# Performance work log

Measured on AMD Instinct MI355X. Metric: run time of the kernel, lower is better.

Reference implementation:

```python
import jax, jax.numpy as jnp
import numpy as np

B, S, C = 8, 512, 1024
H = 16
R = 32            # lora_rank
LORA_ALPHA = 1.0  # lora scaling (alpha=1)
HID = C           # mlp_ratio = 1


def setup_inputs() -> dict:
    key = jax.random.key(0)
    ks = jax.random.split(key, 20)
    g = lambda k, shp, s=0.02: jax.random.normal(k, shp, dtype=jnp.float32) * s
    inp = {
        "x": jax.random.normal(ks[0], (B, S, C), dtype=jnp.float32),
        "mask": jax.random.randint(ks[1], (B, 3 * S), 0, 2).astype(bool),
        # qkv: Linear(dim, 3*dim, bias=False), stored [in, out]
        "qkv_w": g(ks[2], (C, 3 * C)),
        "qkv_la": g(ks[3], (C, R)),
        "qkv_lb": g(ks[4], (R, 3 * C)),
        "proj_w": g(ks[5], (C, C)),
        "proj_b": jnp.zeros((C,), jnp.float32),
        "proj_la": g(ks[6], (C, R)),
        "proj_lb": g(ks[7], (R, C)),
        "fc1_w": g(ks[8], (C, HID)),
        "fc1_b": jnp.zeros((HID,), jnp.float32),
        "fc1_la": g(ks[9], (C, R)),
        "fc1_lb": g(ks[10], (R, HID)),
        "fc2_w": g(ks[11], (HID, C)),
        "fc2_b": jnp.zeros((C,), jnp.float32),
        "fc2_la": g(ks[12], (C, R)),
        "fc2_lb": g(ks[13], (R, C)),
    }
    return inp


def reference(x, mask, qkv_w, qkv_la, qkv_lb, proj_w, proj_b, proj_la, proj_lb,
              fc1_w, fc1_b, fc1_la, fc1_lb, fc2_w, fc2_b, fc2_la, fc2_lb):
    # cross_modality='a', mask_modality='a' (constants)
    b, s, c = x.shape
    hd = c // H
    scale = hd ** (-0.5)

    # fused QKV + LoRA low-rank update
    qkv = x @ qkv_w + ((x @ qkv_la) @ qkv_lb) * LORA_ALPHA      # [B,S,3C]
    qkv = qkv.reshape(b, s, 3, H, hd).transpose(2, 0, 3, 1, 4)  # [3,B,H,S,hd]
    q, k, v = qkv[0] * scale, qkv[1], qkv[2]

    # fp32 QK^T, modality 'a' mask slice, fill -inf, softmax, NaN->0
    attn = jnp.einsum('bhqd,bhkd->bhqk',
                      q.astype(jnp.float32), k.astype(jnp.float32))
    m = mask[:, :s]                                             # 'a' slice
    attn = jnp.where(m[:, None, None, :], attn, -jnp.inf)
    attn = jax.nn.softmax(attn, axis=-1).astype(x.dtype)
    attn = jnp.where(jnp.isnan(attn), jnp.zeros((), x.dtype), attn)

    xo = jnp.einsum('bhqk,bhkd->bhqd', attn, v)                 # [B,H,S,hd]
    xo = xo.transpose(0, 2, 1, 3).reshape(b, s, c)

    # MLP (with LoRA on both fc layers); torch nn.GELU default = exact erf
    h = xo @ fc1_w + fc1_b + ((xo @ fc1_la) @ fc1_lb) * LORA_ALPHA
    h = jax.nn.gelu(h, approximate=False)
    h = h @ fc2_w + fc2_b + ((h @ fc2_la) @ fc2_lb) * LORA_ALPHA
    xo = xo + h

    out = xo @ proj_w + proj_b + ((xo @ proj_la) @ proj_lb) * LORA_ALPHA
    return out
```

## Files before the change

### kernel.cpp

```cpp
#include <hip/hip_runtime.h>

typedef _Float16 f16;
typedef _Float16 f16x8 __attribute__((ext_vector_type(8)));
typedef _Float16 f16x4v __attribute__((ext_vector_type(4)));
typedef float f32x4 __attribute__((ext_vector_type(4)));

#define DEVINL __device__ __forceinline__

DEVINL void gload16(const void* g, void* l) {
  __builtin_amdgcn_global_load_lds(
      (const __attribute__((address_space(1))) void*)g,
      (__attribute__((address_space(3))) void*)l, 16, 0, 0);
}

__global__ __launch_bounds__(256) void weff3(
    const float* __restrict__ W, const float* __restrict__ la,
    const float* __restrict__ lb, f16* __restrict__ WT,
    int N, int K, int scaleCols)
{
  __shared__ float La[64][36];
  __shared__ f16 Ts[64][72];
  int t = threadIdx.x;
  int n0 = blockIdx.x * 64, k0 = blockIdx.y * 64;
  int w = t >> 6, nn = t & 63;
  #pragma unroll
  for (int i = 0; i < 8; ++i) {
    int idx = i * 256 + t;
    int row = idx >> 5, r = idx & 31;
    La[row][r] = la[(size_t)(k0 + row) * 32 + r];
  }
  float lbr[32];
  #pragma unroll
  for (int r = 0; r < 32; ++r) lbr[r] = lb[(size_t)r * N + n0 + nn];
  float scale = (n0 + nn < scaleCols) ? 0.125f : 1.0f;
  __syncthreads();
  float prev = 0.0f;
  #pragma unroll
  for (int i = 0; i < 16; ++i) {
    int k = w * 16 + i;
    float acc = W[(size_t)(k0 + k) * N + n0 + nn];
    #pragma unroll
    for (int rc = 0; rc < 8; ++rc) {
      float4 a4 = *(const float4*)&La[k][rc * 4];
      acc += a4.x * lbr[rc * 4] + a4.y * lbr[rc * 4 + 1] +
             a4.z * lbr[rc * 4 + 2] + a4.w * lbr[rc * 4 + 3];
    }
    acc *= scale;
    if (i & 1) {
      union { f16 h[2]; unsigned u; } pk;
      pk.h[0] = (f16)prev; pk.h[1] = (f16)acc;
      *(unsigned*)&Ts[nn][k - 1] = pk.u;
    } else prev = acc;
  }
  __syncthreads();
  #pragma unroll
  for (int it = 0; it < 2; ++it) {
    int id = it * 256 + t;
    int row = id >> 3, c8 = id & 7;
    f16x8 h = *(const f16x8*)&Ts[row][c8 * 8];
    *(f16x8*)(WT + (size_t)(n0 + row) * K + k0 + c8 * 8) = h;
  }
}

__global__ __launch_bounds__(256) void cvt_f32_f16(const float* __restrict__ in,
                                                   f16* __restrict__ out)
{
  int i = (blockIdx.x * 256 + threadIdx.x) * 4;
  float4 v = *(const float4*)(in + i);
  f16x4v o = {(f16)v.x, (f16)v.y, (f16)v.z, (f16)v.w};
  *(f16x4v*)(out + i) = o;
}

__global__ __launch_bounds__(256) void mask_canon(const unsigned char* __restrict__ m,
                                                  unsigned char* __restrict__ out)
{
  __shared__ int flag;
  if (threadIdx.x == 0) flag = 0;
  __syncthreads();
  int found = 0;
  for (int p = threadIdx.x; p < 12288; p += 256)
    if ((p & 3) && m[p]) found = 1;
  if (found) flag = 1;
  __syncthreads();
  int u8 = flag;
  const int* mi = (const int*)m;
  for (int idx = threadIdx.x; idx < 4096; idx += 256) {
    int b = idx >> 9, k = idx & 511;
    int v = u8 ? (int)m[b * 1536 + k] : mi[b * 1536 + k];
    out[idx] = (unsigned char)(v != 0);
  }
}

template <int EPI>
__global__ __launch_bounds__(256) void gemm128(
    const f16* __restrict__ A, const f16* __restrict__ Bt,
    int M, int N, int K,
    const float* __restrict__ bias, const f16* __restrict__ resid,
    f16* __restrict__ outH, float* __restrict__ outF,
    f16* __restrict__ Qo, f16* __restrict__ Ko, f16* __restrict__ Vto)
{
  __shared__ __align__(16) f16 As[2][128 * 64];
  __shared__ __align__(16) f16 Bs[2][128 * 64];
  int tid = threadIdx.x, wid = tid >> 6, l = tid & 63;
  int lg = l >> 4, lr = l & 15;
  int nbx = gridDim.x;
  int nwg = nbx * gridDim.y;
  int flat = blockIdx.y * nbx + blockIdx.x;
  flat = (flat & 7) * (nwg >> 3) + (flat >> 3);
  int bm = (flat % nbx) * 128, bn = (flat / nbx) * 128;
  int wr = (wid >> 1) * 64, wc = (wid & 1) * 64;
  f32x4 acc[4][4] = {};

  int srow = l >> 3, scol = l & 7;
  int sc8 = (scol ^ srow) * 8;
  const f16* gA = A + (size_t)(bm + wid * 32 + srow) * K + sc8;
  const f16* gB = Bt + (size_t)(bn + wid * 32 + srow) * K + sc8;
  int lo = wid * 32 * 64;

  #pragma unroll
  for (int is = 0; is < 4; ++is) {
    gload16(gA + (size_t)(is * 8) * K, As[0] + lo + is * 8 * 64);
    gload16(gB + (size_t)(is * 8) * K, Bs[0] + lo + is * 8 * 64);
  }
  __syncthreads();

  int nt = K >> 6;
  for (int ts = 0; ts < nt; ++ts) {
    int cur = ts & 1, nxt = cur ^ 1;
    if (ts + 1 < nt) {
      int k1 = (ts + 1) << 6;
      #pragma unroll
      for (int is = 0; is < 4; ++is) {
        gload16(gA + (size_t)(is * 8) * K + k1, As[nxt] + lo + is * 8 * 64);
        gload16(gB + (size_t)(is * 8) * K + k1, Bs[nxt] + lo + is * 8 * 64);
      }
    }
    const f16* Ac = As[cur];
    const f16* Bc = Bs[cur];
    f16x8 af[2][4], bf[2][4];
    int x = lr & 7;
    #pragma unroll
    for (int i = 0; i < 4; ++i) {
      int row = wr + i * 16 + lr;
      af[0][i] = *(const f16x8*)(Ac + row * 64 + ((lg ^ x) * 8));
      af[1][i] = *(const f16x8*)(Ac + row * 64 + (((4 + lg) ^ x) * 8));
    }
    #pragma unroll
    for (int j = 0; j < 4; ++j) {
      int row = wc + j * 16 + lr;
      bf[0][j] = *(const f16x8*)(Bc + row * 64 + ((lg ^ x) * 8));
      bf[1][j] = *(const f16x8*)(Bc + row * 64 + (((4 + lg) ^ x) * 8));
    }
    #pragma unroll
    for (int kk = 0; kk < 2; ++kk)
      #pragma unroll
      for (int i = 0; i < 4; ++i)
        #pragma unroll
        for (int j = 0; j < 4; ++j)
          acc[i][j] = __builtin_amdgcn_mfma_f32_16x16x32_f16(af[kk][i], bf[kk][j], acc[i][j], 0, 0, 0);
    __syncthreads();
  }

  #pragma unroll
  for (int i = 0; i < 4; ++i) {
    #pragma unroll
    for (int j = 0; j < 4; ++j) {
      int n = bn + wc + j * 16 + lr;
      float bv = (EPI >= 1) ? bias[n] : 0.0f;
      #pragma unroll
      for (int r = 0; r < 4; ++r) {
        int m = bm + wr + i * 16 + lg * 4 + r;
        float v = acc[i][j][r];
        if (EPI == 0) {
          int bb = m >> 9, ss = m & 511;
          int which = n >> 10, c = n & 1023, hh = c >> 6, dd = c & 63;
          size_t base = (size_t)(bb * 16 + hh);
          if (which == 0)      Qo[(base * 512 + ss) * 64 + dd] = (f16)v;
          else if (which == 1) Ko[(base * 512 + ss) * 64 + dd] = (f16)v;
          else                 Vto[(base * 64 + dd) * 512 + ss] = (f16)v;
        } else if (EPI == 1) {
          v += bv;
          v = 0.5f * v * (1.0f + erff(v * 0.70710678118654752f));
          outH[(size_t)m * N + n] = (f16)v;
        } else if (EPI == 2) {
          v += bv + (float)resid[(size_t)m * N + n];
          outH[(size_t)m * N + n] = (f16)v;
        } else {
          outF[(size_t)m * N + n] = v + bv;
        }
      }
    }
  }
}

__global__ __launch_bounds__(256) void attn_kernel(
    const f16* __restrict__ Q, const f16* __restrict__ Kc,
    const f16* __restrict__ Vt, const unsigned char* __restrict__ cmask,
    f16* __restrict__ XO)
{
  __shared__ __align__(16) f16 Ks[128 * 64];
  __shared__ __align__(16) f16 Vs[64 * 128];
  __shared__ __align__(16) f16 Ps[4 * 32 * 128];
  int tid = threadIdx.x, w = tid >> 6, l = tid & 63;
  int lg = l >> 4, lr = l & 15;
  int flat = blockIdx.y * 4 + blockIdx.x;
  flat = (flat & 7) * 64 + (flat >> 3);
  int qblk = flat & 3, bh = flat >> 2;
  int b = bh >> 4, h = bh & 15;
  const f16* Qg = Q + (size_t)bh * 512 * 64 + qblk * 128 * 64;
  const f16* Kg = Kc + (size_t)bh * 512 * 64;
  const f16* Vg = Vt + (size_t)bh * 64 * 512;
  const unsigned char* mb = cmask + b * 512;

  f16x8 qf[2][2];
  #pragma unroll
  for (int i = 0; i < 2; ++i)
    #pragma unroll
    for (int kc = 0; kc < 2; ++kc)
      qf[i][kc] = *(const f16x8*)(Qg + (size_t)(w * 32 + i * 16 + lr) * 64 + kc * 32 + lg * 8);

  f32x4 O[2][4] = {};
  float mrow[2][4], lrow[2][4];
  #pragma unroll
  for (int i = 0; i < 2; ++i)
    #pragma unroll
    for (int r = 0; r < 4; ++r) { mrow[i][r] = -1e30f; lrow[i][r] = 0.0f; }

  f16* Pw = Ps + w * 32 * 128;
  int ksrow = l >> 3;
  int ksc = ((l & 7) ^ ksrow) * 8;
  int vrow = l >> 4;
  int v7 = (w * 4 + vrow) & 7;
  int vsc = ((l & 15) ^ v7) * 8;

  for (int kt = 0; kt < 4; ++kt) {
    __syncthreads();
    #pragma unroll
    for (int is = 0; is < 4; ++is)
      gload16(Kg + (size_t)(kt * 128 + is * 32 + w * 8 + ksrow) * 64 + ksc,
              Ks + (is * 32 + w * 8) * 64);
    #pragma unroll
    for (int is = 0; is < 4; ++is)
      gload16(Vg + (size_t)(is * 16 + w * 4 + vrow) * 512 + kt * 128 + vsc,
              Vs + (is * 16 + w * 4) * 128);
    __syncthreads();

    int x = lr & 7;
    f32x4 sc[2][8] = {};
    #pragma unroll
    for (int j = 0; j < 8; ++j) {
      const f16* krow = Ks + (j * 16 + lr) * 64;
      f16x8 kf0 = *(const f16x8*)(krow + ((lg ^ x) * 8));
      f16x8 kf1 = *(const f16x8*)(krow + (((4 + lg) ^ x) * 8));
      sc[0][j] = __builtin_amdgcn_mfma_f32_16x16x32_f16(qf[0][0], kf0, sc[0][j], 0, 0, 0);
      sc[0][j] = __builtin_amdgcn_mfma_f32_16x16x32_f16(qf[0][1], kf1, sc[0][j], 0, 0, 0);
      sc[1][j] = __builtin_amdgcn_mfma_f32_16x16x32_f16(qf[1][0], kf0, sc[1][j], 0, 0, 0);
      sc[1][j] = __builtin_amdgcn_mfma_f32_16x16x32_f16(qf[1][1], kf1, sc[1][j], 0, 0, 0);
    }
    bool keep[8];
    #pragma unroll
    for (int j = 0; j < 8; ++j) keep[j] = mb[kt * 128 + j * 16 + lr] != 0;
    #pragma unroll
    for (int i = 0; i < 2; ++i)
      #pragma unroll
      for (int j = 0; j < 8; ++j)
        #pragma unroll
        for (int r = 0; r < 4; ++r)
          sc[i][j][r] = keep[j] ? sc[i][j][r] : -1e30f;

    #pragma unroll
    for (int i = 0; i < 2; ++i) {
      #pragma unroll
      for (int r = 0; r < 4; ++r) {
        float pm = sc[i][0][r];
        #pragma unroll
        for (int j = 1; j < 8; ++j) pm = fmaxf(pm, sc[i][j][r]);
        pm = fmaxf(pm, __shfl_xor(pm, 1));
        pm = fmaxf(pm, __shfl_xor(pm, 2));
        pm = fmaxf(pm, __shfl_xor(pm, 4));
        pm = fmaxf(pm, __shfl_xor(pm, 8));
        float mn = fmaxf(mrow[i][r], pm);
        float alpha = __expf(mrow[i][r] - mn);
        mrow[i][r] = mn;
        lrow[i][r] *= alpha;
        #pragma unroll
        for (int jd = 0; jd < 4; ++jd) O[i][jd][r] *= alpha;
      }
    }
    #pragma unroll
    for (int i = 0; i < 2; ++i) {
      float rs[4] = {0.f, 0.f, 0.f, 0.f};
      #pragma unroll
      for (int j = 0; j < 8; ++j)
        #pragma unroll
        for (int r = 0; r < 4; ++r) {
          float p = __expf(sc[i][j][r] - mrow[i][r]);
          rs[r] += p;
          int prow = i * 16 + lg * 4 + r;
          int pc = j * 16 + lr;
          Pw[prow * 128 + ((((pc >> 3) ^ (prow & 7)) << 3) | (pc & 7))] = (f16)p;
        }
      #pragma unroll
      for (int r = 0; r < 4; ++r) {
        float s = rs[r];
        s += __shfl_xor(s, 1); s += __shfl_xor(s, 2);
        s += __shfl_xor(s, 4); s += __shfl_xor(s, 8);
        lrow[i][r] += s;
      }
    }
    #pragma unroll
    for (int kk = 0; kk < 4; ++kk) {
      int c0 = ((kk * 4 + lg) ^ x) * 8;
      f16x8 pa0 = *(const f16x8*)(Pw + lr * 128 + c0);
      f16x8 pa1 = *(const f16x8*)(Pw + (16 + lr) * 128 + c0);
      #pragma unroll
      for (int jd = 0; jd < 4; ++jd) {
        f16x8 vb = *(const f16x8*)(Vs + (jd * 16 + lr) * 128 + c0);
        O[0][jd] = __builtin_amdgcn_mfma_f32_16x16x32_f16(pa0, vb, O[0][jd], 0, 0, 0);
        O[1][jd] = __builtin_amdgcn_mfma_f32_16x16x32_f16(pa1, vb, O[1][jd], 0, 0, 0);
      }
    }
  }

  #pragma unroll
  for (int i = 0; i < 2; ++i)
    #pragma unroll
    for (int r = 0; r < 4; ++r) {
      int q = qblk * 128 + w * 32 + i * 16 + lg * 4 + r;
      float inv = 1.0f / lrow[i][r];
      #pragma unroll
      for (int jd = 0; jd < 4; ++jd) {
        int c = h * 64 + jd * 16 + lr;
        XO[((size_t)b * 512 + q) * 1024 + c] = (f16)(O[i][jd][r] * inv);
      }
    }
}

extern "C" void kernel_launch(void* const* d_in, const int* in_sizes, int n_in,
                              void* d_out, int out_size, void* d_ws, size_t ws_size,
                              hipStream_t stream)
{
  (void)in_sizes; (void)n_in; (void)out_size; (void)ws_size;
  const float* x            = (const float*)d_in[0];
  const unsigned char* mask = (const unsigned char*)d_in[1];
  const float* qkv_w   = (const float*)d_in[2];
  const float* qkv_la  = (const float*)d_in[3];
  const float* qkv_lb  = (const float*)d_in[4];
  const float* proj_w  = (const float*)d_in[5];
  const float* proj_b  = (const float*)d_in[6];
  const float* proj_la = (const float*)d_in[7];
  const float* proj_lb = (const float*)d_in[8];
  const float* fc1_w   = (const float*)d_in[9];
  const float* fc1_b   = (const float*)d_in[10];
  const float* fc1_la  = (const float*)d_in[11];
  const float* fc1_lb  = (const float*)d_in[12];
  const float* fc2_w   = (const float*)d_in[13];
  const float* fc2_b   = (const float*)d_in[14];
  const float* fc2_la  = (const float*)d_in[15];
  const float* fc2_lb  = (const float*)d_in[16];
  float* out = (float*)d_out;

  f16* p = (f16*)d_ws;
  f16* WqkvT = p; p += 3072 * 1024;
  f16* W1T   = p; p += 1024 * 1024;
  f16* W2T   = p; p += 1024 * 1024;
  f16* WpT   = p; p += 1024 * 1024;
  f16* Xh    = p; p += 4096 * 1024;
  f16* Qb    = p; p += 128 * 512 * 64;
  f16* Kb    = p; p += 128 * 512 * 64;
  f16* Vt    = p; p += 128 * 64 * 512;
  f16* XO    = p; p += 4096 * 1024;
  unsigned char* cmask = (unsigned char*)p;
  f16* Hb  = Qb;
  f16* XO2 = Xh;

  weff3<<<dim3(48, 16), 256, 0, stream>>>(qkv_w, qkv_la, qkv_lb, WqkvT, 3072, 1024, 1024);
  weff3<<<dim3(16, 16), 256, 0, stream>>>(fc1_w, fc1_la, fc1_lb, W1T, 1024, 1024, 0);
  weff3<<<dim3(16, 16), 256, 0, stream>>>(fc2_w, fc2_la, fc2_lb, W2T, 1024, 1024, 0);
  weff3<<<dim3(16, 16), 256, 0, stream>>>(proj_w, proj_la, proj_lb, WpT, 1024, 1024, 0);
  cvt_f32_f16<<<4096, 256, 0, stream>>>(x, Xh);
  mask_canon<<<1, 256, 0, stream>>>(mask, cmask);

  gemm128<0><<<dim3(32, 24), 256, 0, stream>>>(Xh, WqkvT, 4096, 3072, 1024,
      nullptr, nullptr, nullptr, nullptr, Qb, Kb, Vt);
  attn_kernel<<<dim3(4, 128), 256, 0, stream>>>(Qb, Kb, Vt, cmask, XO);
  gemm128<1><<<dim3(32, 8), 256, 0, stream>>>(XO, W1T, 4096, 1024, 1024,
      fc1_b, nullptr, Hb, nullptr, nullptr, nullptr, nullptr);
  gemm128<2><<<dim3(32, 8), 256, 0, stream>>>(Hb, W2T, 4096, 1024, 1024,
      fc2_b, XO, XO2, nullptr, nullptr, nullptr, nullptr);
  gemm128<3><<<dim3(32, 8), 256, 0, stream>>>(XO2, WpT, 4096, 1024, 1024,
      proj_b, nullptr, nullptr, out, nullptr, nullptr, nullptr);
}
```

Before: 314.4 us.

## Retile GEMMs with BK=32 and BM template, register-prefetch attention K/V

The GEMM is templated on BM with a K-step of 32 instead of 64, which shrinks LDS use and allows three blocks per CU. The three 1024-wide GEMMs switch to 64-row tiles so they launch twice as many workgroups. The XCD-aware block remap is changed, and s_setprio is raised around the MFMA loops. The attention kernel now prefetches the next K/V tile into registers and writes it to swizzled LDS, replacing direct global-to-LDS loads, and gets a two-blocks-per-CU launch bound. Halving the K-step doubles the number of barriers per GEMM, and the smaller tiles reduce data reuse per block.

```diff
diff --git a/kernel.cpp b/kernel.cpp
--- a/kernel.cpp
+++ b/kernel.cpp
@@ -91,78 +91,76 @@
   }
 }
 
-template <int EPI>
-__global__ __launch_bounds__(256) void gemm128(
+template <int EPI, int BM>
+__global__ __launch_bounds__(256, 3) void gemmk(
     const f16* __restrict__ A, const f16* __restrict__ Bt,
     int M, int N, int K,
     const float* __restrict__ bias, const f16* __restrict__ resid,
     f16* __restrict__ outH, float* __restrict__ outF,
     f16* __restrict__ Qo, f16* __restrict__ Ko, f16* __restrict__ Vto)
 {
-  __shared__ __align__(16) f16 As[2][128 * 64];
-  __shared__ __align__(16) f16 Bs[2][128 * 64];
+  constexpr int MF = BM / 32;
+  __shared__ __align__(16) f16 As[2][BM * 32];
+  __shared__ __align__(16) f16 Bs[2][128 * 32];
   int tid = threadIdx.x, wid = tid >> 6, l = tid & 63;
   int lg = l >> 4, lr = l & 15;
   int nbx = gridDim.x;
-  int nwg = nbx * gridDim.y;
   int flat = blockIdx.y * nbx + blockIdx.x;
-  flat = (flat & 7) * (nwg >> 3) + (flat >> 3);
-  int bm = (flat % nbx) * 128, bn = (flat / nbx) * 128;
-  int wr = (wid >> 1) * 64, wc = (wid & 1) * 64;
-  f32x4 acc[4][4] = {};
-
-  int srow = l >> 3, scol = l & 7;
-  int sc8 = (scol ^ srow) * 8;
-  const f16* gA = A + (size_t)(bm + wid * 32 + srow) * K + sc8;
-  const f16* gB = Bt + (size_t)(bn + wid * 32 + srow) * K + sc8;
-  int lo = wid * 32 * 64;
-
-  #pragma unroll
-  for (int is = 0; is < 4; ++is) {
-    gload16(gA + (size_t)(is * 8) * K, As[0] + lo + is * 8 * 64);
-    gload16(gB + (size_t)(is * 8) * K, Bs[0] + lo + is * 8 * 64);
-  }
+  int xcd = flat & 7, idx = flat >> 3;
+  int mc = nbx >> 3;
+  int bm = (xcd * mc + idx % mc) * BM;
+  int bn = (idx / mc) * 128;
+  int wr = (wid >> 1) * (BM / 2), wc = (wid & 1) * 64;
+  f32x4 acc[MF][4] = {};
+
+  int swz = ((l & 3) ^ ((l >> 3) & 3)) * 8;
+  const f16* gA = A + (size_t)(bm + wid * (BM / 4) + (l >> 2)) * K + swz;
+  const f16* gB = Bt + (size_t)(bn + wid * 32 + (l >> 2)) * K + swz;
+  int xr = (lr >> 1) & 3;
+
+  #pragma unroll
+  for (int ig = 0; ig < BM / 64; ++ig)
+    gload16(gA + (size_t)(ig * 16) * K, As[0] + (wid * (BM / 4) + ig * 16) * 32);
+  #pragma unroll
+  for (int ig = 0; ig < 2; ++ig)
+    gload16(gB + (size_t)(ig * 16) * K, Bs[0] + (wid * 32 + ig * 16) * 32);
   __syncthreads();
 
-  int nt = K >> 6;
+  int nt = K >> 5;
   for (int ts = 0; ts < nt; ++ts) {
     int cur = ts & 1, nxt = cur ^ 1;
     if (ts + 1 < nt) {
-      int k1 = (ts + 1) << 6;
-      #pragma unroll
-      for (int is = 0; is < 4; ++is) {
-        gload16(gA + (size_t)(is * 8) * K + k1, As[nxt] + lo + is * 8 * 64);
-        gload16(gB + (size_t)(is * 8) * K + k1, Bs[nxt] + lo + is * 8 * 64);
-      }
+      int k1 = (ts + 1) << 5;
+      #pragma unroll
+      for (int ig = 0; ig < BM / 64; ++ig)
+        gload16(gA + (size_t)(ig * 16) * K + k1, As[nxt] + (wid * (BM / 4) + ig * 16) * 32);
+      #pragma unroll
+      for (int ig = 0; ig < 2; ++ig)
+        gload16(gB + (size_t)(ig * 16) * K + k1, Bs[nxt] + (wid * 32 + ig * 16) * 32);
     }
     const f16* Ac = As[cur];
     const f16* Bc = Bs[cur];
-    f16x8 af[2][4], bf[2][4];
-    int x = lr & 7;
-    #pragma unroll
-    for (int i = 0; i < 4; ++i) {
-      int row = wr + i * 16 + lr;
-      af[0][i] = *(const f16x8*)(Ac + row * 64 + ((lg ^ x) * 8));
-      af[1][i] = *(const f16x8*)(Ac + row * 64 + (((4 + lg) ^ x) * 8));
-    }
+    f16x8 bf[4];
     #pragma unroll
     for (int j = 0; j < 4; ++j) {
       int row = wc + j * 16 + lr;
-      bf[0][j] = *(const f16x8*)(Bc + row * 64 + ((lg ^ x) * 8));
-      bf[1][j] = *(const f16x8*)(Bc + row * 64 + (((4 + lg) ^ x) * 8));
-    }
-    #pragma unroll
-    for (int kk = 0; kk < 2; ++kk)
-      #pragma unroll
-      for (int i = 0; i < 4; ++i)
-        #pragma unroll
-        for (int j = 0; j < 4; ++j)
-          acc[i][j] = __builtin_amdgcn_mfma_f32_16x16x32_f16(af[kk][i], bf[kk][j], acc[i][j], 0, 0, 0);
+      bf[j] = *(const f16x8*)(Bc + row * 32 + ((lg ^ xr) * 8));
+    }
+    __builtin_amdgcn_s_setprio(1);
+    #pragma unroll
+    for (int i = 0; i < MF; ++i) {
+      int row = wr + i * 16 + lr;
+      f16x8 af = *(const f16x8*)(Ac + row * 32 + ((lg ^ xr) * 8));
+      #pragma unroll
+      for (int j = 0; j < 4; ++j)
+        acc[i][j] = __builtin_amdgcn_mfma_f32_16x16x32_f16(af, bf[j], acc[i][j], 0, 0, 0);
+    }
+    __builtin_amdgcn_s_setprio(0);
     __syncthreads();
   }
 
   #pragma unroll
-  for (int i = 0; i < 4; ++i) {
+  for (int i = 0; i < MF; ++i) {
     #pragma unroll
     for (int j = 0; j < 4; ++j) {
       int n = bn + wc + j * 16 + lr;
@@ -193,7 +191,7 @@
   }
 }
 
-__global__ __launch_bounds__(256) void attn_kernel(
+__global__ __launch_bounds__(256, 2) void attn_kernel(
     const f16* __restrict__ Q, const f16* __restrict__ Kc,
     const f16* __restrict__ Vt, const unsigned char* __restrict__ cmask,
     f16* __restrict__ XO)
@@ -227,26 +225,36 @@
     for (int r = 0; r < 4; ++r) { mrow[i][r] = -1e30f; lrow[i][r] = 0.0f; }
 
   f16* Pw = Ps + w * 32 * 128;
-  int ksrow = l >> 3;
-  int ksc = ((l & 7) ^ ksrow) * 8;
-  int vrow = l >> 4;
-  int v7 = (w * 4 + vrow) & 7;
-  int vsc = ((l & 15) ^ v7) * 8;
+
+  int kR = tid >> 3, kC = (tid & 7) * 8;
+  int vR = tid >> 4, vC = (tid & 15) * 8;
+  f16x8 kreg[4], vreg[4];
+  #pragma unroll
+  for (int i = 0; i < 4; ++i) {
+    kreg[i] = *(const f16x8*)(Kg + (size_t)(i * 32 + kR) * 64 + kC);
+    vreg[i] = *(const f16x8*)(Vg + (size_t)(i * 16 + vR) * 512 + vC);
+  }
 
   for (int kt = 0; kt < 4; ++kt) {
+    #pragma unroll
+    for (int i = 0; i < 4; ++i) {
+      int krow = i * 32 + kR;
+      *(f16x8*)(Ks + krow * 64 + (((tid & 7) ^ (krow & 7)) * 8)) = kreg[i];
+      int vrow = i * 16 + vR;
+      *(f16x8*)(Vs + vrow * 128 + (((tid & 15) ^ (vrow & 7)) * 8)) = vreg[i];
+    }
     __syncthreads();
-    #pragma unroll
-    for (int is = 0; is < 4; ++is)
-      gload16(Kg + (size_t)(kt * 128 + is * 32 + w * 8 + ksrow) * 64 + ksc,
-              Ks + (is * 32 + w * 8) * 64);
-    #pragma unroll
-    for (int is = 0; is < 4; ++is)
-      gload16(Vg + (size_t)(is * 16 + w * 4 + vrow) * 512 + kt * 128 + vsc,
-              Vs + (is * 16 + w * 4) * 128);
-    __syncthreads();
+    if (kt < 3) {
+      #pragma unroll
+      for (int i = 0; i < 4; ++i) {
+        kreg[i] = *(const f16x8*)(Kg + (size_t)((kt + 1) * 128 + i * 32 + kR) * 64 + kC);
+        vreg[i] = *(const f16x8*)(Vg + (size_t)(i * 16 + vR) * 512 + (kt + 1) * 128 + vC);
+      }
+    }
 
     int x = lr & 7;
     f32x4 sc[2][8] = {};
+    __builtin_amdgcn_s_setprio(1);
     #pragma unroll
     for (int j = 0; j < 8; ++j) {
       const f16* krow = Ks + (j * 16 + lr) * 64;
@@ -257,6 +265,7 @@
       sc[1][j] = __builtin_amdgcn_mfma_f32_16x16x32_f16(qf[1][0], kf0, sc[1][j], 0, 0, 0);
       sc[1][j] = __builtin_amdgcn_mfma_f32_16x16x32_f16(qf[1][1], kf1, sc[1][j], 0, 0, 0);
     }
+    __builtin_amdgcn_s_setprio(0);
     bool keep[8];
     #pragma unroll
     for (int j = 0; j < 8; ++j) keep[j] = mb[kt * 128 + j * 16 + lr] != 0;
@@ -308,6 +317,7 @@
         lrow[i][r] += s;
       }
     }
+    __builtin_amdgcn_s_setprio(1);
     #pragma unroll
     for (int kk = 0; kk < 4; ++kk) {
       int c0 = ((kk * 4 + lg) ^ x) * 8;
@@ -320,6 +330,8 @@
         O[1][jd] = __builtin_amdgcn_mfma_f32_16x16x32_f16(pa1, vb, O[1][jd], 0, 0, 0);
       }
     }
+    __builtin_amdgcn_s_setprio(0);
+    __syncthreads();
   }
 
   #pragma unroll
@@ -381,13 +393,13 @@
   cvt_f32_f16<<<4096, 256, 0, stream>>>(x, Xh);
   mask_canon<<<1, 256, 0, stream>>>(mask, cmask);
 
-  gemm128<0><<<dim3(32, 24), 256, 0, stream>>>(Xh, WqkvT, 4096, 3072, 1024,
+  gemmk<0, 128><<<dim3(32, 24), 256, 0, stream>>>(Xh, WqkvT, 4096, 3072, 1024,
       nullptr, nullptr, nullptr, nullptr, Qb, Kb, Vt);
   attn_kernel<<<dim3(4, 128), 256, 0, stream>>>(Qb, Kb, Vt, cmask, XO);
-  gemm128<1><<<dim3(32, 8), 256, 0, stream>>>(XO, W1T, 4096, 1024, 1024,
+  gemmk<1, 64><<<dim3(64, 8), 256, 0, stream>>>(XO, W1T, 4096, 1024, 1024,
       fc1_b, nullptr, Hb, nullptr, nullptr, nullptr, nullptr);
-  gemm128<2><<<dim3(32, 8), 256, 0, stream>>>(Hb, W2T, 4096, 1024, 1024,
+  gemmk<2, 64><<<dim3(64, 8), 256, 0, stream>>>(Hb, W2T, 4096, 1024, 1024,
       fc2_b, XO, XO2, nullptr, nullptr, nullptr, nullptr);
-  gemm128<3><<<dim3(32, 8), 256, 0, stream>>>(XO2, WpT, 4096, 1024, 1024,
+  gemmk<3, 64><<<dim3(64, 8), 256, 0, stream>>>(XO2, WpT, 4096, 1024, 1024,
       proj_b, nullptr, nullptr, out, nullptr, nullptr, nullptr);
 }
```

Result: faster. 283.0 us (-10.0%).
